# Kernel optimization log

Hardware: AMD Instinct MI355X
Metric: run time of the kernel (lower is better)

Reference implementation:

```python
import jax, jax.numpy as jnp
import numpy as np

E = 200000     # number of edge-level cells
NADJ = 3200000 # directed up / down adjacency entries (avg degree 16)
F = 64         # input feature dim (== hidden so all layers share dims)
H = 64         # hidden dim
L = 3          # num_layers
B = 64         # number of graphs in batch
C = 10         # num_classes


def setup_inputs() -> dict:
    key = jax.random.key(0)
    ks = jax.random.split(key, 12)
    x = jax.random.normal(ks[0], (E, F), dtype=jnp.float32)
    up_index = jax.random.randint(ks[1], (2, NADJ), 0, E, dtype=jnp.int32)
    up_orient = 2.0 * jax.random.randint(ks[2], (NADJ,), 0, 2).astype(jnp.float32) - 1.0
    down_index = jax.random.randint(ks[3], (2, NADJ), 0, E, dtype=jnp.int32)
    down_orient = 2.0 * jax.random.randint(ks[4], (NADJ,), 0, 2).astype(jnp.float32) - 1.0
    batch = jnp.sort(jax.random.randint(ks[5], (E,), 0, B, dtype=jnp.int32))
    s = 1.0 / np.sqrt(H)
    W_up = jax.random.uniform(ks[6], (L, H, H), minval=-s, maxval=s, dtype=jnp.float32)
    W_down = jax.random.uniform(ks[7], (L, H, H), minval=-s, maxval=s, dtype=jnp.float32)
    W_self = jax.random.uniform(ks[8], (L, H, H), minval=-s, maxval=s, dtype=jnp.float32)
    lin1_w = jax.random.uniform(ks[9], (H, H), minval=-s, maxval=s, dtype=jnp.float32)
    lin1_b = jnp.zeros((H,), jnp.float32)
    lin2_w = jax.random.uniform(ks[10], (C, H), minval=-s, maxval=s, dtype=jnp.float32)
    lin2_b = jnp.zeros((C,), jnp.float32)
    return {"x": x, "up_index": up_index, "up_orient": up_orient,
            "down_index": down_index, "down_orient": down_orient, "batch": batch,
            "W_up": W_up, "W_down": W_down, "W_self": W_self,
            "lin1_w": lin1_w, "lin1_b": lin1_b, "lin2_w": lin2_w, "lin2_b": lin2_b}


def reference(x, up_index, up_orient, down_index, down_orient, batch,
              W_up, W_down, W_self, lin1_w, lin1_b, lin2_w, lin2_b):
    up_src, up_dst = up_index[0], up_index[1]      # message flows src -> dst
    dn_src, dn_dst = down_index[0], down_index[1]
    h = x
    for l in range(L):
        # sign-weighted gather + scatter-sum over upper/lower adjacency
        m_up = jax.ops.segment_sum(h[up_src] * up_orient[:, None], up_dst, num_segments=E)
        m_dn = jax.ops.segment_sum(h[dn_src] * down_orient[:, None], dn_dst, num_segments=E)
        # OrientedConv: act(update_nn(x) + update_up_nn(agg_up) + update_down_nn(agg_down))
        h = jnp.tanh(h @ W_self[l].T + m_up @ W_up[l].T + m_dn @ W_down[l].T)
    # orientation-invariant readout: abs then per-graph segment sum
    pooled = jax.ops.segment_sum(jnp.abs(h), batch, num_segments=B)  # [B, H]
    z = jax.nn.relu(pooled @ lin1_w.T + lin1_b)
    # dropout(p=0.0, eval) is identity
    return z @ lin2_w.T + lin2_b  # [B, C]
```

## Files before the change

kernel.cpp:

```cpp
#include <hip/hip_runtime.h>
#include <hip/hip_bf16.h>

#define H64 64
typedef float float4a __attribute__((ext_vector_type(4)));
typedef float f32x4  __attribute__((ext_vector_type(4)));
typedef short bf16x8 __attribute__((ext_vector_type(8)));

__device__ __forceinline__ unsigned short f2bf(float x) {
    unsigned b = __float_as_uint(x);
    unsigned r = (b + 0x7fffu + ((b >> 16) & 1u)) >> 16;
    return (unsigned short)r;
}

#define SCAN_B 256

#define RPB       1024
#define RPB_SH    10
#define NBKT_MAX  512
#define R1_CHUNK  8192
#define BC_CHUNK  16384

__global__ __launch_bounds__(256) void bcount_kernel(
    const int* __restrict__ up_dst, const int* __restrict__ dn_dst,
    int* __restrict__ bktcnt, int nadj, int E, int nbkt)
{
    __shared__ int lc[NBKT_MAX];
    int t = threadIdx.x;
    for (int i = t; i < nbkt; i += 256) lc[i] = 0;
    __syncthreads();
    long long base = (long long)blockIdx.x * BC_CHUNK;
    long long total = 2LL * nadj;
    for (int i = 0; i < BC_CHUNK / 256; ++i) {
        long long g = base + i * 256 + t;
        if (g < total) {
            int dst2 = (g < nadj) ? up_dst[(int)g] : E + dn_dst[(int)(g - nadj)];
            atomicAdd(&lc[dst2 >> RPB_SH], 1);
        }
    }
    __syncthreads();
    for (int i = t; i < nbkt; i += 256) {
        int c = lc[i];
        if (c) atomicAdd(&bktcnt[i], c);
    }
}

__global__ __launch_bounds__(256) void bscan_kernel(
    const int* __restrict__ bktcnt, int* __restrict__ bstart, int* __restrict__ gcur,
    int nbkt, int total)
{
    __shared__ int s[SCAN_B];
    int t = threadIdx.x;
    int i0 = t * 2;
    int v0 = (i0     < nbkt) ? bktcnt[i0]     : 0;
    int v1 = (i0 + 1 < nbkt) ? bktcnt[i0 + 1] : 0;
    int tsum = v0 + v1;
    s[t] = tsum; __syncthreads();
    for (int off = 1; off < SCAN_B; off <<= 1) {
        int add = (t >= off) ? s[t - off] : 0;
        int cur = s[t];
        __syncthreads();
        s[t] = cur + add;
        __syncthreads();
    }
    int excl = s[t] - tsum;
    if (i0     < nbkt) { bstart[i0]     = excl;      gcur[i0]     = excl; }
    if (i0 + 1 < nbkt) { bstart[i0 + 1] = excl + v0; gcur[i0 + 1] = excl + v0; }
    if (t == 0) bstart[nbkt] = total;
}

__global__ __launch_bounds__(256) void bin_kernel(
    const int* __restrict__ up_index, const float* __restrict__ up_orient,
    const int* __restrict__ dn_index, const float* __restrict__ dn_orient,
    int* __restrict__ gcur, unsigned* __restrict__ binned,
    int nadj, int E, int nbkt)
{
    __shared__ unsigned sval[R1_CHUNK];
    __shared__ unsigned short sbkt[R1_CHUNK];
    __shared__ int lcnt[NBKT_MAX];
    __shared__ int goff[NBKT_MAX];
    __shared__ int lrank[NBKT_MAX];

    int t = threadIdx.x;
    for (int b = t; b < nbkt; b += 256) lcnt[b] = 0;
    __syncthreads();

    long long base = (long long)blockIdx.x * R1_CHUNK;
    int total = 2 * nadj;
    #pragma unroll 4
    for (int i = 0; i < R1_CHUNK / 256; ++i) {
        long long g = base + i * 256 + t;
        int li = i * 256 + t;
        if (g < total) {
            int src, dst2; float orient;
            if (g < nadj) {
                int e = (int)g;
                src = up_index[e]; dst2 = up_index[nadj + e]; orient = up_orient[e];
            } else {
                int e = (int)(g - nadj);
                src = dn_index[e]; dst2 = E + dn_index[nadj + e]; orient = dn_orient[e];
            }
            unsigned v = ((unsigned)src << RPB_SH) | (unsigned)(dst2 & (RPB - 1))
                       | (orient < 0.f ? 0x80000000u : 0u);
            int bk = dst2 >> RPB_SH;
            sval[li] = v;
            sbkt[li] = (unsigned short)bk;
            atomicAdd(&lcnt[bk], 1);
        } else {
            sbkt[li] = 0xFFFFu;
        }
    }
    __syncthreads();
    for (int b = t; b < nbkt; b += 256) {
        int c = lcnt[b];
        lrank[b] = 0;
        if (c > 0) goff[b] = atomicAdd(&gcur[b], c);
    }
    __syncthreads();
    #pragma unroll 4
    for (int i = 0; i < R1_CHUNK / 256; ++i) {
        int li = i * 256 + t;
        unsigned short bk = sbkt[li];
        if (bk != 0xFFFFu) {
            int r = atomicAdd(&lrank[bk], 1);
            binned[goff[bk] + r] = sval[li];
        }
    }
}

__global__ __launch_bounds__(256) void csr_fill2_kernel(
    const unsigned* __restrict__ binned, const int* __restrict__ bstart,
    int* __restrict__ end2, unsigned* __restrict__ packed2, int n2)
{
    __shared__ int lh[RPB];
    __shared__ int lcur[RPB];
    __shared__ int s[SCAN_B];
    int b = blockIdx.x;
    int t = threadIdx.x;
    int s0 = bstart[b], s1 = bstart[b + 1];
    int dbase = b << RPB_SH;

    for (int i = t; i < RPB; i += 256) lh[i] = 0;
    __syncthreads();
    for (int i = s0 + t; i < s1; i += 256) {
        unsigned v = binned[i];
        atomicAdd(&lh[v & (RPB - 1)], 1);
    }
    __syncthreads();

    int i0 = t * 4;
    int c0 = lh[i0], c1 = lh[i0 + 1], c2 = lh[i0 + 2], c3 = lh[i0 + 3];
    int tsum = c0 + c1 + c2 + c3;
    s[t] = tsum; __syncthreads();
    for (int off = 1; off < SCAN_B; off <<= 1) {
        int add = (t >= off) ? s[t - off] : 0;
        int cur = s[t];
        __syncthreads();
        s[t] = cur + add;
        __syncthreads();
    }
    int excl = s[t] - tsum;
    lcur[i0]     = excl;
    lcur[i0 + 1] = excl + c0;
    lcur[i0 + 2] = excl + c0 + c1;
    lcur[i0 + 3] = excl + c0 + c1 + c2;
    int gd = dbase + i0;
    if (gd     < n2) end2[gd]     = s0 + excl + c0;
    if (gd + 1 < n2) end2[gd + 1] = s0 + excl + c0 + c1;
    if (gd + 2 < n2) end2[gd + 2] = s0 + excl + c0 + c1 + c2;
    if (gd + 3 < n2) end2[gd + 3] = s0 + excl + tsum;
    __syncthreads();

    for (int i = s0 + t; i < s1; i += 256) {
        unsigned v = binned[i];
        int d = (int)(v & (RPB - 1));
        int p = atomicAdd(&lcur[d], 1);
        packed2[s0 + p] = (v & 0x80000000u) | ((v >> RPB_SH) & 0x1FFFFFu);
    }
}

#define SCAN_TILE 1024

__global__ __launch_bounds__(256) void hist2_kernel(
    const int* __restrict__ up_dst, const int* __restrict__ dn_dst,
    int* __restrict__ deg2, int nadj, int E)
{
    int g = blockIdx.x * 256 + threadIdx.x;
    if (g < nadj) {
        atomicAdd(&deg2[up_dst[g]], 1);
    } else {
        int e = g - nadj;
        if (e < nadj) atomicAdd(&deg2[E + dn_dst[e]], 1);
    }
}

__global__ __launch_bounds__(256) void scan_partial(
    const int* __restrict__ deg, int* __restrict__ bsums, int n)
{
    __shared__ int s[SCAN_B];
    int t = threadIdx.x;
    int i0 = blockIdx.x * SCAN_TILE + t * 4;
    int sum = 0;
    if (i0 + 3 < n) {
        int4 v = *(const int4*)(deg + i0);
        sum = v.x + v.y + v.z + v.w;
    } else {
        for (int k = 0; k < 4; ++k) if (i0 + k < n) sum += deg[i0 + k];
    }
    s[t] = sum; __syncthreads();
    for (int off = 128; off > 0; off >>= 1) {
        if (t < off) s[t] += s[t + off];
        __syncthreads();
    }
    if (t == 0) bsums[blockIdx.x] = s[0];
}

__global__ __launch_bounds__(256) void scan_bsums_k(int* bsums, int nblk)
{
    __shared__ int s[SCAN_B];
    int t = threadIdx.x;
    int i0 = t * 4;
    int v0 = 0, v1 = 0, v2 = 0, v3 = 0;
    if (i0     < nblk) v0 = bsums[i0];
    if (i0 + 1 < nblk) v1 = bsums[i0 + 1];
    if (i0 + 2 < nblk) v2 = bsums[i0 + 2];
    if (i0 + 3 < nblk) v3 = bsums[i0 + 3];
    int tsum = v0 + v1 + v2 + v3;
    s[t] = tsum; __syncthreads();
    for (int off = 1; off < SCAN_B; off <<= 1) {
        int add = (t >= off) ? s[t - off] : 0;
        int cur = s[t];
        __syncthreads();
        s[t] = cur + add;
        __syncthreads();
    }
    int excl = s[t] - tsum;
    if (i0     < nblk) bsums[i0]     = excl;
    if (i0 + 1 < nblk) bsums[i0 + 1] = excl + v0;
    if (i0 + 2 < nblk) bsums[i0 + 2] = excl + v0 + v1;
    if (i0 + 3 < nblk) bsums[i0 + 3] = excl + v0 + v1 + v2;
}

__global__ __launch_bounds__(256) void scan_final(
    const int* __restrict__ deg, const int* __restrict__ bsums,
    int* __restrict__ outx, int n)
{
    __shared__ int s[SCAN_B];
    int t = threadIdx.x;
    int i0 = blockIdx.x * SCAN_TILE + t * 4;
    int v0 = 0, v1 = 0, v2 = 0, v3 = 0;
    if (i0 + 3 < n) {
        int4 v = *(const int4*)(deg + i0);
        v0 = v.x; v1 = v.y; v2 = v.z; v3 = v.w;
    } else {
        if (i0     < n) v0 = deg[i0];
        if (i0 + 1 < n) v1 = deg[i0 + 1];
        if (i0 + 2 < n) v2 = deg[i0 + 2];
        if (i0 + 3 < n) v3 = deg[i0 + 3];
    }
    int tsum = v0 + v1 + v2 + v3;
    s[t] = tsum; __syncthreads();
    for (int off = 1; off < SCAN_B; off <<= 1) {
        int add = (t >= off) ? s[t - off] : 0;
        int cur = s[t];
        __syncthreads();
        s[t] = cur + add;
        __syncthreads();
    }
    int excl = s[t] - tsum;
    int base = bsums[blockIdx.x] + excl;
    if (i0     < n) outx[i0]     = base;
    if (i0 + 1 < n) outx[i0 + 1] = base + v0;
    if (i0 + 2 < n) outx[i0 + 2] = base + v0 + v1;
    if (i0 + 3 < n) outx[i0 + 3] = base + v0 + v1 + v2;
}

__global__ __launch_bounds__(256) void reorder2_kernel(
    const int* __restrict__ up_index, const float* __restrict__ up_orient,
    const int* __restrict__ dn_index, const float* __restrict__ dn_orient,
    int* __restrict__ end2, unsigned* __restrict__ packed2, int nadj, int E)
{
    int g = blockIdx.x * 256 + threadIdx.x;
    if (g < nadj) {
        int src = up_index[g];
        int dst = up_index[nadj + g];
        int p = atomicAdd(&end2[dst], 1);
        packed2[p] = (unsigned)src | (up_orient[g] < 0.f ? 0x80000000u : 0u);
    } else {
        int e = g - nadj;
        if (e < nadj) {
            int src = dn_index[e];
            int dst = dn_index[nadj + e];
            int p = atomicAdd(&end2[E + dst], 1);
            packed2[p] = (unsigned)src | (dn_orient[e] < 0.f ? 0x80000000u : 0u);
        }
    }
}

__global__ __launch_bounds__(256) void conv_bf16_kernel(
    const float* __restrict__ x, unsigned short* __restrict__ hb, size_t n)
{
    size_t i = ((size_t)blockIdx.x * 256 + threadIdx.x) * 4;
    if (i + 3 < n) {
        float4a v = *(const float4a*)(x + i);
        uint2 o;
        o.x = (unsigned)f2bf(v[0]) | ((unsigned)f2bf(v[1]) << 16);
        o.y = (unsigned)f2bf(v[2]) | ((unsigned)f2bf(v[3]) << 16);
        *(uint2*)(hb + i) = o;
    } else {
        for (size_t k = i; k < n; ++k) hb[k] = f2bf(x[k]);
    }
}

__global__ __launch_bounds__(256) void convW_kernel(
    const float* __restrict__ Ws, const float* __restrict__ Wu,
    const float* __restrict__ Wd, unsigned short* __restrict__ Wb, int L)
{
    int i = blockIdx.x * 256 + threadIdx.x;
    int total = L * 3 * 4096;
    if (i >= total) return;
    int l = i / (3 * 4096);
    int m = (i / 4096) % 3;
    int r = i & 4095;
    const float* src = (m == 0) ? Ws : ((m == 1) ? Wu : Wd);
    Wb[i] = f2bf(src[l * 4096 + r]);
}

__device__ __forceinline__ void seg_sum2(
    const char* __restrict__ hbase, const unsigned* __restrict__ packed2,
    int s0, int s1, unsigned fp4, int g, int lane, float& r0, float& r1)
{
    float a0 = 0.f, a1 = 0.f;
    for (int b = s0; b < s1; b += 64) {
        int cnt = min(64, s1 - b);
        unsigned pk = (lane < cnt) ? packed2[b + lane] : 0u;
        int n = 0;
        for (; n + 16 <= cnt; n += 16) {
            unsigned p[8], u[8];
            #pragma unroll
            for (int t = 0; t < 8; ++t) p[t] = __shfl(pk, n + 2 * t + g);
            #pragma unroll
            for (int t = 0; t < 8; ++t)
                u[t] = *(const unsigned*)(hbase + ((p[t] << 7) + fp4));
            #pragma unroll
            for (int t = 0; t < 8; ++t) {
                float sgn = ((int)p[t] < 0) ? -1.f : 1.f;
                a0 = fmaf(__uint_as_float(u[t] << 16),         sgn, a0);
                a1 = fmaf(__uint_as_float(u[t] & 0xFFFF0000u), sgn, a1);
            }
        }
        for (; n + 8 <= cnt; n += 8) {
            unsigned p[4], u[4];
            #pragma unroll
            for (int t = 0; t < 4; ++t) p[t] = __shfl(pk, n + 2 * t + g);
            #pragma unroll
            for (int t = 0; t < 4; ++t)
                u[t] = *(const unsigned*)(hbase + ((p[t] << 7) + fp4));
            #pragma unroll
            for (int t = 0; t < 4; ++t) {
                float sgn = ((int)p[t] < 0) ? -1.f : 1.f;
                a0 = fmaf(__uint_as_float(u[t] << 16),         sgn, a0);
                a1 = fmaf(__uint_as_float(u[t] & 0xFFFF0000u), sgn, a1);
            }
        }
        for (; n < cnt; n += 2) {
            int idx = n + g;
            unsigned pe = __shfl(pk, min(idx, cnt - 1));
            float sgn = (idx < cnt) ? (((int)pe < 0) ? -1.f : 1.f) : 0.f;
            unsigned u = *(const unsigned*)(hbase + ((pe << 7) + fp4));
            a0 = fmaf(__uint_as_float(u << 16),         sgn, a0);
            a1 = fmaf(__uint_as_float(u & 0xFFFF0000u), sgn, a1);
        }
    }
    r0 = a0; r1 = a1;
}

__global__ __launch_bounds__(256) void gather_kernel(
    const unsigned* __restrict__ hb32,
    const int* __restrict__ end2, const unsigned* __restrict__ packed2,
    unsigned* __restrict__ mup32, unsigned* __restrict__ mdn32, int E)
{
    int dst = (int)((blockIdx.x * 256u + threadIdx.x) >> 6);
    if (dst >= E) return;
    int lane = threadIdx.x & 63;
    int g  = lane >> 5;
    unsigned fp = lane & 31;
    unsigned fp4 = fp * 4;
    const char* hbase = (const char*)hb32;

    int s0U = (dst == 0) ? 0 : end2[dst - 1];
    int s1U = end2[dst];
    float u0, u1;
    seg_sum2(hbase, packed2, s0U, s1U, fp4, g, lane, u0, u1);

    int s0D = end2[E + dst - 1];
    int s1D = end2[E + dst];
    float d0, d1;
    seg_sum2(hbase, packed2, s0D, s1D, fp4, g, lane, d0, d1);

    u0 += __shfl_xor(u0, 32); u1 += __shfl_xor(u1, 32);
    d0 += __shfl_xor(d0, 32); d1 += __shfl_xor(d1, 32);

    unsigned valU = (unsigned)f2bf(u0) | ((unsigned)f2bf(u1) << 16);
    unsigned valD = (unsigned)f2bf(d0) | ((unsigned)f2bf(d1) << 16);
    unsigned* ptr = g ? mdn32 : mup32;
    ptr[(size_t)dst * 32 + fp] = g ? valD : valU;
}

__global__ __launch_bounds__(256) void gemm_tanh_mfma(
    const unsigned short* __restrict__ hbin,
    const unsigned short* __restrict__ mupb, const unsigned short* __restrict__ mdnb,
    const unsigned short* __restrict__ Wb,
    unsigned short* __restrict__ hbout, int E, int nblk16)
{
    int wid  = (blockIdx.x * 256 + threadIdx.x) >> 6;
    if (wid >= nblk16) return;
    int lane = threadIdx.x & 63;
    int lg = lane >> 4;
    int lr = lane & 15;

    bf16x8 bfr[3][4][2];
    #pragma unroll
    for (int m = 0; m < 3; ++m)
        #pragma unroll
        for (int jt = 0; jt < 4; ++jt)
            #pragma unroll
            for (int ks = 0; ks < 2; ++ks)
                bfr[m][jt][ks] = *(const bf16x8*)(Wb + m * 4096 + (jt * 16 + lr) * 64 + ks * 32 + lg * 8);

    int base = wid * 16;
    int arow = base + lr;
    bool ok = (arow < E);
    size_t aoff = (size_t)arow * H64 + lg * 8;

    bf16x8 afr[3][2];
    bf16x8 zz = {0, 0, 0, 0, 0, 0, 0, 0};
    #pragma unroll
    for (int ks = 0; ks < 2; ++ks) {
        afr[0][ks] = ok ? *(const bf16x8*)(hbin + aoff + ks * 32) : zz;
        afr[1][ks] = ok ? *(const bf16x8*)(mupb + aoff + ks * 32) : zz;
        afr[2][ks] = ok ? *(const bf16x8*)(mdnb + aoff + ks * 32) : zz;
    }

    f32x4 acc[4];
    #pragma unroll
    for (int jt = 0; jt < 4; ++jt) acc[jt] = (f32x4){0.f, 0.f, 0.f, 0.f};

    #pragma unroll
    for (int m = 0; m < 3; ++m)
        #pragma unroll
        for (int ks = 0; ks < 2; ++ks)
            #pragma unroll
            for (int jt = 0; jt < 4; ++jt)
                acc[jt] = __builtin_amdgcn_mfma_f32_16x16x32_bf16(
                    afr[m][ks], bfr[m][jt][ks], acc[jt], 0, 0, 0);

    #pragma unroll
    for (int jt = 0; jt < 4; ++jt) {
        #pragma unroll
        for (int reg = 0; reg < 4; ++reg) {
            int row = base + lg * 4 + reg;
            if (row < E) {
                float v = acc[jt][reg];
                float e2 = __expf(2.f * v);
                float val = 1.f - 2.f / (e2 + 1.f);
                hbout[(size_t)row * H64 + jt * 16 + lr] = f2bf(val);
            }
        }
    }
}

#define ROWS_PER_WAVE 64
__global__ __launch_bounds__(256) void pool_kernel(
    const unsigned short* __restrict__ hb, const int* __restrict__ batch,
    float* __restrict__ pooled, int E)
{
    int wave = (int)((blockIdx.x * 256 + threadIdx.x) >> 6);
    int j = threadIdx.x & 63;
    int row0 = wave * ROWS_PER_WAVE;
    if (row0 >= E) return;
    int row1 = min(row0 + ROWS_PER_WAVE, E);

    int cur = batch[row0];
    float acc = 0.f;
    for (int i = row0; i < row1; ++i) {
        int b = batch[i];
        if (b != cur) {
            atomicAdd(&pooled[(size_t)cur * H64 + j], acc);
            acc = 0.f;
            cur = b;
        }
        unsigned u = hb[(size_t)i * H64 + j];
        acc += fabsf(__uint_as_float(u << 16));
    }
    atomicAdd(&pooled[(size_t)cur * H64 + j], acc);
}

__global__ __launch_bounds__(64) void head_kernel(
    const float* __restrict__ pooled,
    const float* __restrict__ lin1_w, const float* __restrict__ lin1_b,
    const float* __restrict__ lin2_w, const float* __restrict__ lin2_b,
    float* __restrict__ out, int C)
{
    __shared__ float p[64];
    __shared__ float z[64];
    int b = blockIdx.x;
    int t = threadIdx.x;

    p[t] = pooled[(size_t)b * H64 + t];
    __syncthreads();

    float acc = lin1_b[t];
    #pragma unroll
    for (int k = 0; k < 64; ++k) acc += p[k] * lin1_w[t * 64 + k];
    z[t] = fmaxf(acc, 0.f);
    __syncthreads();

    if (t < C) {
        float o = lin2_b[t];
        #pragma unroll
        for (int k = 0; k < 64; ++k) o += z[k] * lin2_w[t * 64 + k];
        out[(size_t)b * C + t] = o;
    }
}

extern "C" void kernel_launch(void* const* d_in, const int* in_sizes, int n_in,
                              void* d_out, int out_size, void* d_ws, size_t ws_size,
                              hipStream_t stream)
{
    const float* x          = (const float*)d_in[0];
    const int*   up_index   = (const int*)  d_in[1];
    const float* up_orient  = (const float*)d_in[2];
    const int*   down_index = (const int*)  d_in[3];
    const float* down_orient= (const float*)d_in[4];
    const int*   batch      = (const int*)  d_in[5];
    const float* W_up       = (const float*)d_in[6];
    const float* W_down     = (const float*)d_in[7];
    const float* W_self     = (const float*)d_in[8];
    const float* lin1_w     = (const float*)d_in[9];
    const float* lin1_b     = (const float*)d_in[10];
    const float* lin2_w     = (const float*)d_in[11];
    const float* lin2_b     = (const float*)d_in[12];
    float* out = (float*)d_out;

    const int E    = in_sizes[0] / H64;
    const int NADJ = in_sizes[1] / 2;
    const int C    = in_sizes[11] / H64;
    const int B    = out_size / C;
    const int L    = in_sizes[6] / (H64 * H64);

    unsigned short* hb      = (unsigned short*)d_ws;
    unsigned short* mupb    = hb   + (size_t)E * H64;
    unsigned short* mdnb    = mupb + (size_t)E * H64;
    float*          pooled  = (float*)(mdnb + (size_t)E * H64);
    int*            end2    = (int*)(pooled + (size_t)B * H64);
    int*            deg2    = end2 + (size_t)2 * E;
    int*            bsums   = deg2 + (size_t)2 * E;
    int*            bktcnt  = bsums + 1024;
    int*            gcur    = bktcnt + NBKT_MAX;
    int*            bstart  = gcur + NBKT_MAX;
    unsigned short* Wb      = (unsigned short*)(bstart + NBKT_MAX + 1);
    unsigned*       packed2 = (unsigned*)(Wb + (size_t)L * 3 * 4096);
    unsigned*       binned  = packed2 + (size_t)2 * NADJ;

    const int n2    = 2 * E;
    const int nbkt  = (n2 + RPB - 1) >> RPB_SH;
    const int total = 2 * NADJ;
    const int gather_blocks = (int)(((long long)E * 64 + 255) / 256);
    const int conv_blocks   = (int)(((long long)E * H64 / 4 + 255) / 256);
    const int nblk16        = (E + 15) / 16;
    const int gemm_blocks   = (nblk16 + 3) / 4;
    const int convw_blocks  = (L * 3 * 4096 + 255) / 256;
    const int pool_waves    = (E + ROWS_PER_WAVE - 1) / ROWS_PER_WAVE;
    const int pool_blocks   = (pool_waves + 3) / 4;

    if (nbkt <= NBKT_MAX) {
        const int bc_blocks = (total + BC_CHUNK - 1) / BC_CHUNK;
        const int r1_blocks = (total + R1_CHUNK - 1) / R1_CHUNK;
        hipMemsetAsync(bktcnt, 0, (size_t)NBKT_MAX * sizeof(int), stream);
        bcount_kernel<<<bc_blocks, 256, 0, stream>>>(up_index + NADJ, down_index + NADJ,
                                                     bktcnt, NADJ, E, nbkt);
        bscan_kernel<<<1, 256, 0, stream>>>(bktcnt, bstart, gcur, nbkt, total);
        bin_kernel<<<r1_blocks, 256, 0, stream>>>(up_index, up_orient, down_index, down_orient,
                                                  gcur, binned, NADJ, E, nbkt);
        csr_fill2_kernel<<<nbkt, 256, 0, stream>>>(binned, bstart, end2, packed2, n2);
    } else {
        const int both_blocks = (total + 255) / 256;
        const int nscan = (n2 + SCAN_TILE - 1) / SCAN_TILE;
        hipMemsetAsync(deg2, 0, (size_t)n2 * sizeof(int), stream);
        hist2_kernel<<<both_blocks, 256, 0, stream>>>(up_index + NADJ, down_index + NADJ, deg2, NADJ, E);
        scan_partial<<<nscan, 256, 0, stream>>>(deg2, bsums, n2);
        scan_bsums_k<<<1, 256, 0, stream>>>(bsums, nscan);
        scan_final<<<nscan, 256, 0, stream>>>(deg2, bsums, end2, n2);
        reorder2_kernel<<<both_blocks, 256, 0, stream>>>(up_index, up_orient, down_index, down_orient,
                                                         end2, packed2, NADJ, E);
    }

    conv_bf16_kernel<<<conv_blocks, 256, 0, stream>>>(x, hb, (size_t)E * H64);
    convW_kernel<<<convw_blocks, 256, 0, stream>>>(W_self, W_up, W_down, Wb, L);

    for (int l = 0; l < L; ++l) {
        gather_kernel<<<gather_blocks, 256, 0, stream>>>(
            (const unsigned*)hb, end2, packed2,
            (unsigned*)mupb, (unsigned*)mdnb, E);
        gemm_tanh_mfma<<<gemm_blocks, 256, 0, stream>>>(
            hb, mupb, mdnb, Wb + (size_t)l * 3 * 4096, hb, E, nblk16);
    }

    hipMemsetAsync(pooled, 0, (size_t)B * H64 * sizeof(float), stream);
    pool_kernel<<<pool_blocks, 256, 0, stream>>>(hb, batch, pooled, E);
    head_kernel<<<B, 64, 0, stream>>>(pooled, lin1_w, lin1_b, lin2_w, lin2_b, out, C);
}
```

Before: 770.2 us.

## Interleave up/down gathers for short segments and halve bucket row span

Adds a fast path in the gather kernel that processes the up and down adjacency segments in one interleaved loop when both have at most 64 entries, issuing both sets of row loads together to raise memory-level parallelism. The original unrolled per-segment loops become a simple fallback for long segments. The CSR-building pass is retuned to 512 rows per bucket with twice as many buckets, and the scan kernels are adjusted to match. The price is extra predication on padded iterations where one segment is shorter than the other.

Result: faster. 731.5 us (-5.0%).

```diff
diff --git a/kernel.cpp b/kernel.cpp
--- a/kernel.cpp
+++ b/kernel.cpp
@@ -14,9 +14,9 @@
 
 #define SCAN_B 256
 
-#define RPB       1024
-#define RPB_SH    10
-#define NBKT_MAX  512
+#define RPB       512
+#define RPB_SH    9
+#define NBKT_MAX  1024
 #define R1_CHUNK  8192
 #define BC_CHUNK  16384
 
@@ -50,10 +50,12 @@
 {
     __shared__ int s[SCAN_B];
     int t = threadIdx.x;
-    int i0 = t * 2;
+    int i0 = t * 4;
     int v0 = (i0     < nbkt) ? bktcnt[i0]     : 0;
     int v1 = (i0 + 1 < nbkt) ? bktcnt[i0 + 1] : 0;
-    int tsum = v0 + v1;
+    int v2 = (i0 + 2 < nbkt) ? bktcnt[i0 + 2] : 0;
+    int v3 = (i0 + 3 < nbkt) ? bktcnt[i0 + 3] : 0;
+    int tsum = v0 + v1 + v2 + v3;
     s[t] = tsum; __syncthreads();
     for (int off = 1; off < SCAN_B; off <<= 1) {
         int add = (t >= off) ? s[t - off] : 0;
@@ -63,8 +65,10 @@
         __syncthreads();
     }
     int excl = s[t] - tsum;
-    if (i0     < nbkt) { bstart[i0]     = excl;      gcur[i0]     = excl; }
-    if (i0 + 1 < nbkt) { bstart[i0 + 1] = excl + v0; gcur[i0 + 1] = excl + v0; }
+    if (i0     < nbkt) { bstart[i0]     = excl;                gcur[i0]     = excl; }
+    if (i0 + 1 < nbkt) { bstart[i0 + 1] = excl + v0;           gcur[i0 + 1] = excl + v0; }
+    if (i0 + 2 < nbkt) { bstart[i0 + 2] = excl + v0 + v1;      gcur[i0 + 2] = excl + v0 + v1; }
+    if (i0 + 3 < nbkt) { bstart[i0 + 3] = excl + v0 + v1 + v2; gcur[i0 + 3] = excl + v0 + v1 + v2; }
     if (t == 0) bstart[nbkt] = total;
 }
 
@@ -147,9 +151,9 @@
     }
     __syncthreads();
 
-    int i0 = t * 4;
-    int c0 = lh[i0], c1 = lh[i0 + 1], c2 = lh[i0 + 2], c3 = lh[i0 + 3];
-    int tsum = c0 + c1 + c2 + c3;
+    int i0 = t * 2;
+    int c0 = lh[i0], c1 = lh[i0 + 1];
+    int tsum = c0 + c1;
     s[t] = tsum; __syncthreads();
     for (int off = 1; off < SCAN_B; off <<= 1) {
         int add = (t >= off) ? s[t - off] : 0;
@@ -161,13 +165,9 @@
     int excl = s[t] - tsum;
     lcur[i0]     = excl;
     lcur[i0 + 1] = excl + c0;
-    lcur[i0 + 2] = excl + c0 + c1;
-    lcur[i0 + 3] = excl + c0 + c1 + c2;
     int gd = dbase + i0;
     if (gd     < n2) end2[gd]     = s0 + excl + c0;
-    if (gd + 1 < n2) end2[gd + 1] = s0 + excl + c0 + c1;
-    if (gd + 2 < n2) end2[gd + 2] = s0 + excl + c0 + c1 + c2;
-    if (gd + 3 < n2) end2[gd + 3] = s0 + excl + tsum;
+    if (gd + 1 < n2) end2[gd + 1] = s0 + excl + tsum;
     __syncthreads();
 
     for (int i = s0 + t; i < s1; i += 256) {
@@ -325,48 +325,19 @@
     Wb[i] = f2bf(src[l * 4096 + r]);
 }
 
-__device__ __forceinline__ void seg_sum2(
-    const char* __restrict__ hbase, const unsigned* __restrict__ packed2,
-    int s0, int s1, unsigned fp4, int g, int lane, float& r0, float& r1)
+__device__ __forceinline__ void seg_sum2_slow(
+    const unsigned* __restrict__ hb32, const unsigned* __restrict__ packed2,
+    int s0, int s1, unsigned fp, int g, int lane, float& r0, float& r1)
 {
     float a0 = 0.f, a1 = 0.f;
     for (int b = s0; b < s1; b += 64) {
         int cnt = min(64, s1 - b);
         unsigned pk = (lane < cnt) ? packed2[b + lane] : 0u;
-        int n = 0;
-        for (; n + 16 <= cnt; n += 16) {
-            unsigned p[8], u[8];
-            #pragma unroll
-            for (int t = 0; t < 8; ++t) p[t] = __shfl(pk, n + 2 * t + g);
-            #pragma unroll
-            for (int t = 0; t < 8; ++t)
-                u[t] = *(const unsigned*)(hbase + ((p[t] << 7) + fp4));
-            #pragma unroll
-            for (int t = 0; t < 8; ++t) {
-                float sgn = ((int)p[t] < 0) ? -1.f : 1.f;
-                a0 = fmaf(__uint_as_float(u[t] << 16),         sgn, a0);
-                a1 = fmaf(__uint_as_float(u[t] & 0xFFFF0000u), sgn, a1);
-            }
-        }
-        for (; n + 8 <= cnt; n += 8) {
-            unsigned p[4], u[4];
-            #pragma unroll
-            for (int t = 0; t < 4; ++t) p[t] = __shfl(pk, n + 2 * t + g);
-            #pragma unroll
-            for (int t = 0; t < 4; ++t)
-                u[t] = *(const unsigned*)(hbase + ((p[t] << 7) + fp4));
-            #pragma unroll
-            for (int t = 0; t < 4; ++t) {
-                float sgn = ((int)p[t] < 0) ? -1.f : 1.f;
-                a0 = fmaf(__uint_as_float(u[t] << 16),         sgn, a0);
-                a1 = fmaf(__uint_as_float(u[t] & 0xFFFF0000u), sgn, a1);
-            }
-        }
-        for (; n < cnt; n += 2) {
+        for (int n = 0; n < cnt; n += 2) {
             int idx = n + g;
             unsigned pe = __shfl(pk, min(idx, cnt - 1));
             float sgn = (idx < cnt) ? (((int)pe < 0) ? -1.f : 1.f) : 0.f;
-            unsigned u = *(const unsigned*)(hbase + ((pe << 7) + fp4));
+            unsigned u = hb32[(pe << 5) + fp];
             a0 = fmaf(__uint_as_float(u << 16),         sgn, a0);
             a1 = fmaf(__uint_as_float(u & 0xFFFF0000u), sgn, a1);
         }
@@ -384,18 +355,48 @@
     int lane = threadIdx.x & 63;
     int g  = lane >> 5;
     unsigned fp = lane & 31;
-    unsigned fp4 = fp * 4;
-    const char* hbase = (const char*)hb32;
 
     int s0U = (dst == 0) ? 0 : end2[dst - 1];
     int s1U = end2[dst];
-    float u0, u1;
-    seg_sum2(hbase, packed2, s0U, s1U, fp4, g, lane, u0, u1);
-
     int s0D = end2[E + dst - 1];
     int s1D = end2[E + dst];
-    float d0, d1;
-    seg_sum2(hbase, packed2, s0D, s1D, fp4, g, lane, d0, d1);
+    int cntU = s1U - s0U, cntD = s1D - s0D;
+
+    float u0, u1, d0, d1;
+    if (cntU <= 64 && cntD <= 64) {
+        int limU = max(cntU - 1, 0), limD = max(cntD - 1, 0);
+        unsigned pkU = (cntU > 0) ? packed2[s0U + min(lane, limU)] : 0u;
+        unsigned pkD = (cntD > 0) ? packed2[s0D + min(lane, limD)] : 0u;
+        float a0 = 0.f, a1 = 0.f, b0 = 0.f, b1 = 0.f;
+        int nmax = max(cntU, cntD);
+        for (int n = 0; n < nmax; n += 8) {
+            unsigned pU[4], pD[4], vU[4], vD[4];
+            float sU[4], sD[4];
+            #pragma unroll
+            for (int t = 0; t < 4; ++t) {
+                int idx = n + 2 * t + g;
+                pU[t] = __shfl(pkU, min(idx, limU));
+                pD[t] = __shfl(pkD, min(idx, limD));
+                sU[t] = (idx < cntU) ? (((int)pU[t] < 0) ? -1.f : 1.f) : 0.f;
+                sD[t] = (idx < cntD) ? (((int)pD[t] < 0) ? -1.f : 1.f) : 0.f;
+            }
+            #pragma unroll
+            for (int t = 0; t < 4; ++t) vU[t] = hb32[(pU[t] << 5) + fp];
+            #pragma unroll
+            for (int t = 0; t < 4; ++t) vD[t] = hb32[(pD[t] << 5) + fp];
+            #pragma unroll
+            for (int t = 0; t < 4; ++t) {
+                a0 = fmaf(__uint_as_float(vU[t] << 16),         sU[t], a0);
+                a1 = fmaf(__uint_as_float(vU[t] & 0xFFFF0000u), sU[t], a1);
+                b0 = fmaf(__uint_as_float(vD[t] << 16),         sD[t], b0);
+                b1 = fmaf(__uint_as_float(vD[t] & 0xFFFF0000u), sD[t], b1);
+            }
+        }
+        u0 = a0; u1 = a1; d0 = b0; d1 = b1;
+    } else {
+        seg_sum2_slow(hb32, packed2, s0U, s1U, fp, g, lane, u0, u1);
+        seg_sum2_slow(hb32, packed2, s0D, s1D, fp, g, lane, d0, d1);
+    }
 
     u0 += __shfl_xor(u0, 32); u1 += __shfl_xor(u1, 32);
     d0 += __shfl_xor(d0, 32); d1 += __shfl_xor(d1, 32);
```
